# Kernel tuning notes

Measured on AMD Instinct MI355X. Metric: run time of the kernel, lower is better.

The kernel has to match this reference:

```python
import jax, jax.numpy as jnp
import numpy as np

MAX_DIM = 1024
VOCAB = 257
DEPTH = 6
Q_DIM = MAX_DIM // 4  # 256
EXP_DIMS = [1, 2, 4, 8, 16, 32, 64, 128]  # expander sizes: current_q doubles up to Q_DIM
BATCH, SEQ = 8, 4096


def qlinear(q, W):
    """Quaternion Hamilton-product linear.
    q: [..., in, 4] (last dim = r,i,j,k components), W: [4, out, in] (stacked r,i,j,k weights).
    Returns [..., out, 4].
    """
    # P[..., o, w, a] = F.linear(component_a, W_w)  -> all 16 small GEMMs in one einsum
    P = jnp.einsum('...ia,woi->...owa', q, W)
    Pr, Pi, Pj, Pk = P[..., 0, :], P[..., 1, :], P[..., 2, :], P[..., 3, :]  # each [..., out, 4]
    out_r = Pr[..., 0] - Pi[..., 1] - Pj[..., 2] - Pk[..., 3]
    out_i = Pi[..., 0] + Pr[..., 1] + Pk[..., 2] - Pj[..., 3]
    out_j = Pj[..., 0] - Pk[..., 1] + Pr[..., 2] + Pi[..., 3]
    out_k = Pk[..., 0] + Pj[..., 1] - Pi[..., 2] + Pr[..., 3]
    return jnp.stack([out_r, out_i, out_j, out_k], axis=-1)


def qnormalize(q):
    norm = jnp.linalg.norm(q, axis=-1, keepdims=True)
    return q / (norm + 1e-8)


def setup_inputs() -> dict:
    key = jax.random.key(0)
    ks = jax.random.split(key, 4 + len(EXP_DIMS))
    inp = {}
    inp['x'] = jax.random.randint(ks[0], (BATCH, SEQ), 0, VOCAB)
    inp['emb'] = jax.random.normal(ks[1], (VOCAB, 4), dtype=jnp.float32)
    for idx, cq in enumerate(EXP_DIMS):
        scale = cq ** (-0.5)
        inp[f'w_exp{idx}'] = jax.random.uniform(ks[2 + idx], (4, cq, cq), jnp.float32, -scale, scale)
    scale = Q_DIM ** (-0.5)
    inp['w_layers'] = jax.random.uniform(ks[-2], (DEPTH, 4, Q_DIM, Q_DIM), jnp.float32, -scale, scale)
    inp['w_head'] = jax.random.normal(ks[-1], (VOCAB, MAX_DIM), dtype=jnp.float32) * MAX_DIM ** (-0.5)
    return inp


def reference(x, emb, w_exp0, w_exp1, w_exp2, w_exp3, w_exp4, w_exp5, w_exp6, w_exp7,
              w_layers, w_head):
    q = emb[x][:, :, None, :]  # [B, S, 1, 4]
    for w in (w_exp0, w_exp1, w_exp2, w_exp3, w_exp4, w_exp5, w_exp6, w_exp7):
        delta = jnp.tanh(qlinear(q, w))
        q = jnp.concatenate([q + delta, q - delta], axis=2)  # doubles quaternion dim
    for d in range(DEPTH):
        q = qnormalize(qlinear(q, w_layers[d]))
    stability_loss = jnp.mean(jnp.abs(q[..., 0]))
    h_flat = q.reshape(x.shape[0], x.shape[1], -1)  # [B, S, MAX_DIM]
    logits = jnp.einsum('bsd,vd->bsv', h_flat, w_head)
    return (logits, stability_loss)
```

## Files before the change

kernel.cpp:

```cpp
#include <hip/hip_runtime.h>


typedef _Float16 f16x8 __attribute__((ext_vector_type(8)));
typedef float    f32x4 __attribute__((ext_vector_type(4)));

#define GL2LDS16(gp, lp) __builtin_amdgcn_global_load_lds(                     \
    (const __attribute__((address_space(1))) void*)(gp),                       \
    (__attribute__((address_space(3))) void*)(lp), 16, 0, 0)

__device__ __forceinline__ unsigned short f2h(float f) {
  union { _Float16 h; unsigned short u; } c;
  c.h = (_Float16)f;
  return c.u;
}
__device__ __forceinline__ float h2f(unsigned short u) {
  union { unsigned short u; _Float16 h; } c;
  c.u = u;
  return (float)c.h;
}

__device__ __forceinline__ void expand_one(const float* __restrict__ w,
                                           unsigned short* __restrict__ out,
                                           int cq, int kbits, int id) {
  const int K = 1 << kbits;
  const int n = id >> kbits;
  const int k = id & (K - 1);
  float val = 0.f;
  if (n < 4 * cq) {
    const int o = n >> 2, a = n & 3, i = k >> 2, b = k & 3;
    const int   comp[4][4] = {{0,1,2,3},{1,0,3,2},{2,3,0,1},{3,2,1,0}};
    const float sgn [4][4] = {{1.f,-1.f,-1.f,-1.f},{1.f,1.f,1.f,-1.f},
                              {1.f,-1.f,1.f,1.f},{1.f,1.f,-1.f,1.f}};
    val = sgn[a][b] * w[comp[a][b] * cq * cq + o * cq + i];
  }
  out[id] = f2h(val);
}

__global__ __launch_bounds__(256) void prep_weights(
    const float* __restrict__ we4, const float* __restrict__ we5,
    const float* __restrict__ we6, const float* __restrict__ we7,
    const float* __restrict__ wlay, const float* __restrict__ wh,
    unsigned short* __restrict__ E4, unsigned short* __restrict__ E5,
    unsigned short* __restrict__ E6, unsigned short* __restrict__ E7,
    unsigned short* __restrict__ EL, unsigned short* __restrict__ WH) {
  const int b = blockIdx.x;
  const int tid = threadIdx.x;
  if (b < 32) {
    expand_one(we4, E4, 16, 6, b * 256 + tid);
  } else if (b < 96) {
    expand_one(we5, E5, 32, 7, (b - 32) * 256 + tid);
  } else if (b < 352) {
    expand_one(we6, E6, 64, 8, (b - 96) * 256 + tid);
  } else if (b < 1376) {
    expand_one(we7, E7, 128, 9, (b - 352) * 256 + tid);
  } else if (b < 25952) {
    const int d = (b - 1376) >> 12;
    const int id = ((b - 1376) & 4095) * 256 + tid;
    expand_one(wlay + (size_t)d * 262144, EL + (size_t)d * 1048576, 256, 10,
               id);
  } else {
    const int id = (b - 25952) * 256 + tid;
    const int v = id >> 10, k = id & 1023;
    WH[id] = f2h(v < 257 ? wh[v * 1024 + k] : 0.f);
  }
}

template <int CQ>
__device__ __forceinline__ void exp_step(float (&q)[16][4],
                                         const float* __restrict__ w) {
  float d[CQ][4];
#pragma unroll
  for (int o = 0; o < CQ; o++) {
    float pr = 0.f, pi = 0.f, pj = 0.f, pk = 0.f;
#pragma unroll
    for (int i = 0; i < CQ; i++) {
      const float wr = w[0 * CQ * CQ + o * CQ + i];
      const float wi = w[1 * CQ * CQ + o * CQ + i];
      const float wj = w[2 * CQ * CQ + o * CQ + i];
      const float wk = w[3 * CQ * CQ + o * CQ + i];
      const float qr = q[i][0], qi = q[i][1], qj = q[i][2], qk = q[i][3];
      pr += wr * qr - wi * qi - wj * qj - wk * qk;
      pi += wi * qr + wr * qi + wk * qj - wj * qk;
      pj += wj * qr - wk * qi + wr * qj + wi * qk;
      pk += wk * qr + wj * qi - wi * qj + wr * qk;
    }
    d[o][0] = tanhf(pr); d[o][1] = tanhf(pi);
    d[o][2] = tanhf(pj); d[o][3] = tanhf(pk);
  }
#pragma unroll
  for (int o = 0; o < CQ; o++)
#pragma unroll
    for (int a = 0; a < 4; a++) {
      const float dd = d[o][a], qq = q[o][a];
      q[o][a]      = qq + dd;
      q[CQ + o][a] = qq - dd;
    }
}

__global__ __launch_bounds__(256) void embed_expand(
    const int* __restrict__ x, const float* __restrict__ emb,
    const float* __restrict__ w0, const float* __restrict__ w1,
    const float* __restrict__ w2, const float* __restrict__ w3,
    unsigned short* __restrict__ out) {
  const int t = blockIdx.x * 256 + threadIdx.x;
  float q[16][4];
  const int v = x[t];
  const float4 e = *(const float4*)(emb + v * 4);
  q[0][0] = e.x; q[0][1] = e.y; q[0][2] = e.z; q[0][3] = e.w;
  exp_step<1>(q, w0);
  exp_step<2>(q, w1);
  exp_step<4>(q, w2);
  exp_step<8>(q, w3);
  ushort4* o4 = (ushort4*)(out + (size_t)t * 64);
#pragma unroll
  for (int c = 0; c < 16; c++) {
    ushort4 u;
    u.x = f2h(q[c][0]); u.y = f2h(q[c][1]);
    u.z = f2h(q[c][2]); u.w = f2h(q[c][3]);
    o4[c] = u;
  }
}

template <int EPI>
__global__ __launch_bounds__(256) void gemm_epi(
    const unsigned short* __restrict__ W,
    const unsigned short* __restrict__ Act,
    unsigned short* __restrict__ OutB, float* __restrict__ OutF,
    int K, int Nreal, int ldout) {
  __shared__ unsigned short WtL[2][4096];
  __shared__ unsigned short WtH[2][4096];
  __shared__ unsigned short AtL[2][4096];
  __shared__ unsigned short AtH[2][4096];
  __shared__ float lsum[4];

  const int tid  = threadIdx.x;
  const int wave = tid >> 6;
  const int lane = tid & 63;
  const int l15  = lane & 15;
  const int quad = lane >> 4;

  const int Gx = gridDim.x;
  const int L  = blockIdx.y * Gx + blockIdx.x;
  const int j  = L & 7;
  const int s  = L >> 3;
  const int nblock = (s % Gx) * 128;
  const int mblock = (32 * j + s / Gx) * 128;
  const int wn = (wave & 1) * 64;
  const int wm = (wave >> 1) * 64;

  f32x4 acc[4][4];
  const f32x4 zero = {0.f, 0.f, 0.f, 0.f};
#pragma unroll
  for (int a = 0; a < 4; a++)
#pragma unroll
    for (int b = 0; b < 4; b++) acc[a][b] = zero;

  const int row0 = tid >> 2;
  const int sub  = tid & 3;
  const unsigned short* gW0 = W   + (size_t)(nblock + row0)      * K + sub * 8;
  const unsigned short* gW1 = W   + (size_t)(nblock + row0 + 64) * K + sub * 8;
  const unsigned short* gA0 = Act + (size_t)(mblock + row0)      * K + sub * 8;
  const unsigned short* gA1 = Act + (size_t)(mblock + row0 + 64) * K + sub * 8;
  const int lofs0 = wave * 512;
  const int lofs1 = 2048 + wave * 512;

  const int NIT = K >> 6;

  GL2LDS16(gW0,      &WtL[0][lofs0]);
  GL2LDS16(gW1,      &WtL[0][lofs1]);
  GL2LDS16(gW0 + 32, &WtH[0][lofs0]);
  GL2LDS16(gW1 + 32, &WtH[0][lofs1]);
  GL2LDS16(gA0,      &AtL[0][lofs0]);
  GL2LDS16(gA1,      &AtL[0][lofs1]);
  GL2LDS16(gA0 + 32, &AtH[0][lofs0]);
  GL2LDS16(gA1 + 32, &AtH[0][lofs1]);

  for (int it = 0; it < NIT; it++) {
    const int cur = it & 1, nxt = cur ^ 1;
    __syncthreads();
    if (it + 1 < NIT) {
      const int kb = (it + 1) * 64;
      GL2LDS16(gW0 + kb,      &WtL[nxt][lofs0]);
      GL2LDS16(gW1 + kb,      &WtL[nxt][lofs1]);
      GL2LDS16(gW0 + kb + 32, &WtH[nxt][lofs0]);
      GL2LDS16(gW1 + kb + 32, &WtH[nxt][lofs1]);
      GL2LDS16(gA0 + kb,      &AtL[nxt][lofs0]);
      GL2LDS16(gA1 + kb,      &AtL[nxt][lofs1]);
      GL2LDS16(gA0 + kb + 32, &AtH[nxt][lofs0]);
      GL2LDS16(gA1 + kb + 32, &AtH[nxt][lofs1]);
    }
    {
      f16x8 afr[4], bfr[4];
#pragma unroll
      for (int tn = 0; tn < 4; tn++)
        afr[tn] =
            *(const f16x8*)&WtL[cur][(wn + tn * 16 + l15) * 32 + quad * 8];
#pragma unroll
      for (int tm = 0; tm < 4; tm++)
        bfr[tm] =
            *(const f16x8*)&AtL[cur][(wm + tm * 16 + l15) * 32 + quad * 8];
#pragma unroll
      for (int tn = 0; tn < 4; tn++)
#pragma unroll
        for (int tm = 0; tm < 4; tm++)
          acc[tn][tm] = __builtin_amdgcn_mfma_f32_16x16x32_f16(
              afr[tn], bfr[tm], acc[tn][tm], 0, 0, 0);
    }
    {
      f16x8 afr[4], bfr[4];
#pragma unroll
      for (int tn = 0; tn < 4; tn++)
        afr[tn] =
            *(const f16x8*)&WtH[cur][(wn + tn * 16 + l15) * 32 + quad * 8];
#pragma unroll
      for (int tm = 0; tm < 4; tm++)
        bfr[tm] =
            *(const f16x8*)&AtH[cur][(wm + tm * 16 + l15) * 32 + quad * 8];
#pragma unroll
      for (int tn = 0; tn < 4; tn++)
#pragma unroll
        for (int tm = 0; tm < 4; tm++)
          acc[tn][tm] = __builtin_amdgcn_mfma_f32_16x16x32_f16(
              afr[tn], bfr[tm], acc[tn][tm], 0, 0, 0);
    }
  }

  if constexpr (EPI == 0) {
#pragma unroll
    for (int tn = 0; tn < 4; tn++) {
      const int n = nblock + wn + tn * 16 + quad * 4;
      if (n < Nreal) {
#pragma unroll
        for (int tm = 0; tm < 4; tm++) {
          const int token = mblock + wm + tm * 16 + l15;
          const f32x4 v = acc[tn][tm];
          const unsigned short* ip = Act + (size_t)token * K + n;
          const float i0 = h2f(ip[0]), i1 = h2f(ip[1]);
          const float i2 = h2f(ip[2]), i3 = h2f(ip[3]);
          const float d0 = tanhf(v[0]), d1 = tanhf(v[1]);
          const float d2 = tanhf(v[2]), d3 = tanhf(v[3]);
          ushort4 up, um;
          up.x = f2h(i0 + d0); up.y = f2h(i1 + d1);
          up.z = f2h(i2 + d2); up.w = f2h(i3 + d3);
          um.x = f2h(i0 - d0); um.y = f2h(i1 - d1);
          um.z = f2h(i2 - d2); um.w = f2h(i3 - d3);
          *(ushort4*)&OutB[(size_t)token * ldout + n] = up;
          *(ushort4*)&OutB[(size_t)token * ldout + Nreal + n] = um;
        }
      }
    }
  } else if constexpr (EPI == 1 || EPI == 2) {
    float loss = 0.f;
#pragma unroll
    for (int tn = 0; tn < 4; tn++) {
      const int n = nblock + wn + tn * 16 + quad * 4;
#pragma unroll
      for (int tm = 0; tm < 4; tm++) {
        const int token = mblock + wm + tm * 16 + l15;
        const f32x4 v = acc[tn][tm];
        const float nrm =
            sqrtf(v[0] * v[0] + v[1] * v[1] + v[2] * v[2] + v[3] * v[3]);
        const float inv = 1.f / (nrm + 1e-8f);
        ushort4 u;
        u.x = f2h(v[0] * inv); u.y = f2h(v[1] * inv);
        u.z = f2h(v[2] * inv); u.w = f2h(v[3] * inv);
        *(ushort4*)&OutB[(size_t)token * ldout + n] = u;
        if constexpr (EPI == 2) loss += fabsf(v[0] * inv);
      }
    }
    if constexpr (EPI == 2) {
#pragma unroll
      for (int off = 32; off > 0; off >>= 1) loss += __shfl_down(loss, off);
      if (lane == 0) lsum[wave] = loss;
      __syncthreads();
      if (tid == 0)
        atomicAdd(OutF,
                  (lsum[0] + lsum[1] + lsum[2] + lsum[3]) * (1.f / 8388608.f));
    }
  } else {
#pragma unroll
    for (int tn = 0; tn < 4; tn++) {
      const int n = nblock + wn + tn * 16 + quad * 4;
      if (n < 257) {
#pragma unroll
        for (int tm = 0; tm < 4; tm++) {
          const int token = mblock + wm + tm * 16 + l15;
          const f32x4 v = acc[tn][tm];
#pragma unroll
          for (int r = 0; r < 4; r++)
            if (n + r < 257) OutF[(size_t)token * 257 + n + r] = v[r];
        }
      }
    }
  }
}

extern "C" void kernel_launch(void* const* d_in, const int* in_sizes, int n_in,
                              void* d_out, int out_size, void* d_ws,
                              size_t ws_size, hipStream_t stream) {
  const int*   x    = (const int*)d_in[0];
  const float* emb  = (const float*)d_in[1];
  const float* we0  = (const float*)d_in[2];
  const float* we1  = (const float*)d_in[3];
  const float* we2  = (const float*)d_in[4];
  const float* we3  = (const float*)d_in[5];
  const float* we4  = (const float*)d_in[6];
  const float* we5  = (const float*)d_in[7];
  const float* we6  = (const float*)d_in[8];
  const float* we7  = (const float*)d_in[9];
  const float* wlay = (const float*)d_in[10];
  const float* wh   = (const float*)d_in[11];
  float* out = (float*)d_out;

  char* p = (char*)d_ws;
  auto alloc = [&](size_t bytes) {
    void* r = (void*)p;
    p += (bytes + 255) & ~(size_t)255;
    return r;
  };
  unsigned short* act0 = (unsigned short*)alloc(32768ull * 1024 * 2);
  unsigned short* act1 = (unsigned short*)alloc(32768ull * 1024 * 2);
  unsigned short* E4 = (unsigned short*)alloc(128 * 64 * 2);
  unsigned short* E5 = (unsigned short*)alloc(128 * 128 * 2);
  unsigned short* E6 = (unsigned short*)alloc(256 * 256 * 2);
  unsigned short* E7 = (unsigned short*)alloc(512 * 512 * 2);
  unsigned short* EL = (unsigned short*)alloc(6ull * 1024 * 1024 * 2);
  unsigned short* WH = (unsigned short*)alloc(384 * 1024 * 2);

  hipMemsetAsync(out + 8421376, 0, 4, stream);

  prep_weights<<<dim3(27488), 256, 0, stream>>>(we4, we5, we6, we7, wlay, wh,
                                                E4, E5, E6, E7, EL, WH);

  embed_expand<<<dim3(128), 256, 0, stream>>>(x, emb, we0, we1, we2, we3, act0);

  gemm_epi<0><<<dim3(1, 256), 256, 0, stream>>>(E4, act0, act1, nullptr, 64,
                                                64, 128);
  gemm_epi<0><<<dim3(1, 256), 256, 0, stream>>>(E5, act1, act0, nullptr, 128,
                                                128, 256);
  gemm_epi<0><<<dim3(2, 256), 256, 0, stream>>>(E6, act0, act1, nullptr, 256,
                                                256, 512);
  gemm_epi<0><<<dim3(4, 256), 256, 0, stream>>>(E7, act1, act0, nullptr, 512,
                                                512, 1024);

  unsigned short* a = act0;
  unsigned short* b = act1;
  for (int d = 0; d < 5; d++) {
    gemm_epi<1><<<dim3(8, 256), 256, 0, stream>>>(EL + (size_t)d * 1048576, a,
                                                  b, nullptr, 1024, 1024, 1024);
    unsigned short* t = a; a = b; b = t;
  }
  gemm_epi<2><<<dim3(8, 256), 256, 0, stream>>>(EL + 5ull * 1048576, a, b,
                                                out + 8421376, 1024, 1024,
                                                1024);
  { unsigned short* t = a; a = b; b = t; }

  gemm_epi<3><<<dim3(3, 256), 256, 0, stream>>>(WH, a, nullptr, out, 1024, 257,
                                                0);
}
```

Before: 882.1 us.

## Pre-swizzle weights into MFMA fragment order and load them directly from global

Weight matrices are written in prep into a tiled layout matching the 16x32 MFMA A-fragment, so each lane reads its f16x8 fragment straight from global memory (L2-resident) instead of staging weights through LDS. The activation tile keeps LDS staging but gains an XOR swizzle on the k-chunk to cut bank conflicts, and launch bounds request 3 blocks per CU now that LDS use is halved. This trades LDS traffic and occupancy limits for global load latency on the weight path, which is no longer double-buffered ahead of the MFMAs.

```diff
diff --git a/kernel.cpp b/kernel.cpp
--- a/kernel.cpp
+++ b/kernel.cpp
@@ -17,6 +17,11 @@
   union { unsigned short u; _Float16 h; } c;
   c.u = u;
   return (float)c.h;
+}
+
+__device__ __forceinline__ int swz(int n, int k, int K) {
+  return (((n >> 4) * (K >> 5) + (k >> 5)) << 9) | (((k >> 3) & 3) << 7) |
+         ((n & 15) << 3) | (k & 7);
 }
 
 __device__ __forceinline__ void expand_one(const float* __restrict__ w,
@@ -33,7 +38,7 @@
                               {1.f,-1.f,1.f,1.f},{1.f,1.f,-1.f,1.f}};
     val = sgn[a][b] * w[comp[a][b] * cq * cq + o * cq + i];
   }
-  out[id] = f2h(val);
+  out[swz(n, k, K)] = f2h(val);
 }
 
 __global__ __launch_bounds__(256) void prep_weights(
@@ -61,7 +66,7 @@
   } else {
     const int id = (b - 25952) * 256 + tid;
     const int v = id >> 10, k = id & 1023;
-    WH[id] = f2h(v < 257 ? wh[v * 1024 + k] : 0.f);
+    WH[swz(v, k, 1024)] = f2h(v < 257 ? wh[v * 1024 + k] : 0.f);
   }
 }
 
@@ -122,13 +127,11 @@
 }
 
 template <int EPI>
-__global__ __launch_bounds__(256) void gemm_epi(
+__global__ __launch_bounds__(256, 3) void gemm_epi(
     const unsigned short* __restrict__ W,
     const unsigned short* __restrict__ Act,
     unsigned short* __restrict__ OutB, float* __restrict__ OutF,
     int K, int Nreal, int ldout) {
-  __shared__ unsigned short WtL[2][4096];
-  __shared__ unsigned short WtH[2][4096];
   __shared__ unsigned short AtL[2][4096];
   __shared__ unsigned short AtH[2][4096];
   __shared__ float lsum[4];
@@ -156,20 +159,27 @@
     for (int b = 0; b < 4; b++) acc[a][b] = zero;
 
   const int row0 = tid >> 2;
-  const int sub  = tid & 3;
-  const unsigned short* gW0 = W   + (size_t)(nblock + row0)      * K + sub * 8;
-  const unsigned short* gW1 = W   + (size_t)(nblock + row0 + 64) * K + sub * 8;
+  const int sub  = (tid & 3) ^ ((row0 >> 1) & 3);
   const unsigned short* gA0 = Act + (size_t)(mblock + row0)      * K + sub * 8;
   const unsigned short* gA1 = Act + (size_t)(mblock + row0 + 64) * K + sub * 8;
   const int lofs0 = wave * 512;
   const int lofs1 = 2048 + wave * 512;
 
+  const unsigned short* wp[4];
+#pragma unroll
+  for (int tn = 0; tn < 4; tn++)
+    wp[tn] = W +
+             ((size_t)(((nblock + wn) >> 4) + tn) * (K >> 5)) * 512 + lane * 8;
+
+  int aoff[4];
+#pragma unroll
+  for (int tm = 0; tm < 4; tm++) {
+    const int r = wm + tm * 16 + l15;
+    aoff[tm] = r * 32 + ((quad ^ ((r >> 1) & 3)) << 3);
+  }
+
   const int NIT = K >> 6;
 
-  GL2LDS16(gW0,      &WtL[0][lofs0]);
-  GL2LDS16(gW1,      &WtL[0][lofs1]);
-  GL2LDS16(gW0 + 32, &WtH[0][lofs0]);
-  GL2LDS16(gW1 + 32, &WtH[0][lofs1]);
   GL2LDS16(gA0,      &AtL[0][lofs0]);
   GL2LDS16(gA1,      &AtL[0][lofs1]);
   GL2LDS16(gA0 + 32, &AtH[0][lofs0]);
@@ -180,49 +190,36 @@
     __syncthreads();
     if (it + 1 < NIT) {
       const int kb = (it + 1) * 64;
-      GL2LDS16(gW0 + kb,      &WtL[nxt][lofs0]);
-      GL2LDS16(gW1 + kb,      &WtL[nxt][lofs1]);
-      GL2LDS16(gW0 + kb + 32, &WtH[nxt][lofs0]);
-      GL2LDS16(gW1 + kb + 32, &WtH[nxt][lofs1]);
       GL2LDS16(gA0 + kb,      &AtL[nxt][lofs0]);
       GL2LDS16(gA1 + kb,      &AtL[nxt][lofs1]);
       GL2LDS16(gA0 + kb + 32, &AtH[nxt][lofs0]);
       GL2LDS16(gA1 + kb + 32, &AtH[nxt][lofs1]);
     }
-    {
-      f16x8 afr[4], bfr[4];
-#pragma unroll
-      for (int tn = 0; tn < 4; tn++)
-        afr[tn] =
-            *(const f16x8*)&WtL[cur][(wn + tn * 16 + l15) * 32 + quad * 8];
+    f16x8 wfrL[4], wfrH[4];
+#pragma unroll
+    for (int tn = 0; tn < 4; tn++) {
+      wfrL[tn] = *(const f16x8*)(wp[tn]);
+      wfrH[tn] = *(const f16x8*)(wp[tn] + 512);
+      wp[tn] += 1024;
+    }
+    f16x8 bfrL[4], bfrH[4];
+#pragma unroll
+    for (int tm = 0; tm < 4; tm++) {
+      bfrL[tm] = *(const f16x8*)&AtL[cur][aoff[tm]];
+      bfrH[tm] = *(const f16x8*)&AtH[cur][aoff[tm]];
+    }
+#pragma unroll
+    for (int tn = 0; tn < 4; tn++)
 #pragma unroll
       for (int tm = 0; tm < 4; tm++)
-        bfr[tm] =
-            *(const f16x8*)&AtL[cur][(wm + tm * 16 + l15) * 32 + quad * 8];
-#pragma unroll
-      for (int tn = 0; tn < 4; tn++)
-#pragma unroll
-        for (int tm = 0; tm < 4; tm++)
-          acc[tn][tm] = __builtin_amdgcn_mfma_f32_16x16x32_f16(
-              afr[tn], bfr[tm], acc[tn][tm], 0, 0, 0);
-    }
-    {
-      f16x8 afr[4], bfr[4];
-#pragma unroll
-      for (int tn = 0; tn < 4; tn++)
-        afr[tn] =
-            *(const f16x8*)&WtH[cur][(wn + tn * 16 + l15) * 32 + quad * 8];
+        acc[tn][tm] = __builtin_amdgcn_mfma_f32_16x16x32_f16(
+            wfrL[tn], bfrL[tm], acc[tn][tm], 0, 0, 0);
+#pragma unroll
+    for (int tn = 0; tn < 4; tn++)
 #pragma unroll
       for (int tm = 0; tm < 4; tm++)
-        bfr[tm] =
-            *(const f16x8*)&AtH[cur][(wm + tm * 16 + l15) * 32 + quad * 8];
-#pragma unroll
-      for (int tn = 0; tn < 4; tn++)
-#pragma unroll
-        for (int tm = 0; tm < 4; tm++)
-          acc[tn][tm] = __builtin_amdgcn_mfma_f32_16x16x32_f16(
-              afr[tn], bfr[tm], acc[tn][tm], 0, 0, 0);
-    }
+        acc[tn][tm] = __builtin_amdgcn_mfma_f32_16x16x32_f16(
+            wfrH[tn], bfrH[tm], acc[tn][tm], 0, 0, 0);
   }
 
   if constexpr (EPI == 0) {
```

After: 900.4 us. 1.02x slower.
